# Kernel optimization log

Hardware: AMD Instinct MI355X
Metric: run time of the kernel (lower is better)

The kernel has to match this reference:

```python
import jax, jax.numpy as jnp
import numpy as np

B, L = 1, 384
D_EDGE, D_BIAS, N_HEAD, D_HEAD = 128, 64, 4, 48
INF = 1000000.0
SCALE = 1.0 / np.sqrt(D_HEAD)
EPS = 1e-5


def _layernorm(x, g, b):
    mu = jnp.mean(x, axis=-1, keepdims=True)
    var = jnp.mean(jnp.square(x - mu), axis=-1, keepdims=True)
    return (x - mu) * jax.lax.rsqrt(var + EPS) * g + b


def _rope(x, pos):
    # x: [B, n, L, h, d], pos: [B, L] integer positions along the attended (i/j) axis
    half = x.shape[-1] // 2
    inv_freq = 1.0 / (10000.0 ** (jnp.arange(half, dtype=jnp.float32) / half))
    ang = pos.astype(jnp.float32)[..., None] * inv_freq          # [B, L, half]
    cos = jnp.cos(ang)[:, None, :, None, :]                       # [B,1,L,1,half]
    sin = jnp.sin(ang)[:, None, :, None, :]
    x1, x2 = jnp.split(x, 2, axis=-1)
    return jnp.concatenate([x1 * cos - x2 * sin, x1 * sin + x2 * cos], axis=-1)


def setup_inputs() -> dict:
    key = jax.random.key(0)
    ks = jax.random.split(key, 10)
    s = 0.02
    return {
        "edge": jax.random.normal(ks[0], (B, L, L, D_EDGE), jnp.float32),
        "bias": jax.random.normal(ks[1], (B, L, L, D_BIAS), jnp.float32),
        "edge_pos": jnp.arange(B * L, dtype=jnp.int32).reshape(B, L),
        "edge_mask": jnp.ones((B, L, L), jnp.float32),
        "ln_e_g": jnp.ones((D_EDGE,), jnp.float32),
        "ln_e_b": jnp.zeros((D_EDGE,), jnp.float32),
        "ln_b_g": jnp.ones((D_BIAS,), jnp.float32),
        "ln_b_b": jnp.zeros((D_BIAS,), jnp.float32),
        "Wq": jax.random.normal(ks[2], (D_EDGE, N_HEAD * D_HEAD), jnp.float32) * s,
        "Wk": jax.random.normal(ks[3], (D_EDGE, N_HEAD * D_HEAD), jnp.float32) * s,
        "Wv": jax.random.normal(ks[4], (D_EDGE, N_HEAD * D_HEAD), jnp.float32) * s,
        "Wb": jax.random.normal(ks[5], (D_BIAS, N_HEAD), jnp.float32) * s,
        "Wg": jax.random.normal(ks[6], (D_EDGE, N_HEAD * D_HEAD), jnp.float32) * s,
        "bg": jnp.zeros((N_HEAD * D_HEAD,), jnp.float32),
        "Wo": jax.random.normal(ks[7], (N_HEAD * D_HEAD, D_EDGE), jnp.float32) * s,
    }


def reference(edge, bias, edge_pos, edge_mask, ln_e_g, ln_e_b, ln_b_g, ln_b_b,
              Wq, Wk, Wv, Wb, Wg, bg, Wo):
    # is_row=True: swap the two residue axes of the pair representation
    e = jnp.transpose(edge, (0, 2, 1, 3))
    bi = jnp.transpose(bias, (0, 2, 1, 3))
    e = _layernorm(e, ln_e_g, ln_e_b)
    bi = _layernorm(bi, ln_b_g, ln_b_b)

    def proj(x, W):
        return (x @ W).reshape(B, L, L, N_HEAD, D_HEAD)

    q = proj(e, Wq)                      # [B, n, i, h, d]
    k = proj(e, Wk)
    v = proj(e, Wv)
    q = _rope(q, edge_pos)
    k = _rope(k, edge_pos)
    b_h = bi @ Wb                        # [B, i, j, h]
    gate = jax.nn.sigmoid(proj(e, Wg) + bg.reshape(1, 1, 1, N_HEAD, D_HEAD))

    q = q * SCALE
    k = k / L
    attn = jnp.einsum('bnihk,bnjhk->bijh', q, k) + b_h
    attn = jax.nn.softmax(attn, axis=-2)                 # softmax over j (dim -2)
    attn = attn + (INF * (edge_mask - 1.0))[..., None]    # post-softmax additive mask

    out = jnp.einsum('bijh,bnjhd->bnihd', attn, v)        # [B, n, i, h, d]
    out = gate * out
    out = out.reshape(B, L, L, N_HEAD * D_HEAD) @ Wo      # [B, n, i, d_edge]
    return jnp.transpose(out, (0, 2, 1, 3))               # undo row permute
```

## Files before the change

kernel.cpp:

```cpp
#include <hip/hip_runtime.h>
#include <hip/hip_bf16.h>


#define LQ 384
#define DE 128
#define DBI 64
#define NH 4
#define DH 48
#define NPOS (LQ*LQ)
#define KQK (LQ*DH)

typedef __attribute__((ext_vector_type(8))) short short8;
typedef __attribute__((ext_vector_type(4))) float f32x4;
typedef unsigned short u16;
typedef unsigned int u32;

__device__ __forceinline__ float b2f(u16 u) {
  union { u32 i; float f; } v; v.i = ((u32)u) << 16; return v.f;
}
__device__ __forceinline__ u16 f2b(float f) {
  __hip_bfloat16 h = __float2bfloat16(f);
  return __builtin_bit_cast(unsigned short, h);
}
__device__ __forceinline__ float wred_sum(float v) {
  #pragma unroll
  for (int o = 32; o; o >>= 1) v += __shfl_down(v, o);
  return __shfl(v, 0);
}

__device__ __forceinline__ void gemm_128x192(
    const u16* __restrict__ A, long lda, const u16* __restrict__ B, long ldb,
    int kTiles, u16* sA, u16* sB, f32x4 (&acc)[4][6])
{
  const int t = threadIdx.x;
  const int w = t >> 6, lane = t & 63, quad = lane >> 4, l16 = lane & 15;
  const int wr = w >> 1, wc = w & 1;
  for (int kt = 0; kt < kTiles; ++kt) {
    #pragma unroll
    for (int r = 0; r < 4; ++r) {
      int id = t + r * 256, row = id >> 3, c8 = (id & 7) * 8;
      *(uint4*)(sA + row * 72 + c8) = *(const uint4*)(A + (long)row * lda + kt * 64 + c8);
    }
    #pragma unroll
    for (int r = 0; r < 6; ++r) {
      int id = t + r * 256, row = id >> 3, c8 = (id & 7) * 8;
      *(uint4*)(sB + row * 72 + c8) = *(const uint4*)(B + (long)row * ldb + kt * 64 + c8);
    }
    __syncthreads();
    #pragma unroll
    for (int kk = 0; kk < 64; kk += 32) {
      short8 a[4], bf[6];
      #pragma unroll
      for (int rr = 0; rr < 4; ++rr)
        a[rr] = *(const short8*)(sA + (wr * 64 + rr * 16 + l16) * 72 + kk + quad * 8);
      #pragma unroll
      for (int f = 0; f < 6; ++f)
        bf[f] = *(const short8*)(sB + (wc * 96 + f * 16 + l16) * 72 + kk + quad * 8);
      #pragma unroll
      for (int rr = 0; rr < 4; ++rr)
        #pragma unroll
        for (int f = 0; f < 6; ++f)
          acc[rr][f] = __builtin_amdgcn_mfma_f32_16x16x32_bf16(a[rr], bf[f], acc[rr][f], 0, 0, 0);
    }
    __syncthreads();
  }
}

__global__ __launch_bounds__(256) void k_prep_w(
    const float* __restrict__ Wq, const float* __restrict__ Wk,
    const float* __restrict__ Wv, const float* __restrict__ Wg,
    const float* __restrict__ Wo, const int* __restrict__ epos,
    u16* __restrict__ WT, u16* __restrict__ WoT,
    float* __restrict__ cosT, float* __restrict__ sinT)
{
  int idx = blockIdx.x * 256 + threadIdx.x;
  if (idx < 768 * 128) {
    int col = idx >> 7, c = idx & 127;
    int which = col / 192, wi = col % 192;
    const float* W = (which == 0) ? Wq : (which == 1) ? Wk : (which == 2) ? Wv : Wg;
    WT[(long)col * 128 + c] = f2b(W[(long)c * 192 + wi]);
  }
  if (idx < 128 * 192) {
    int c = idx / 192, col = idx % 192;
    WoT[(long)c * 192 + col] = f2b(Wo[(long)col * 128 + c]);
  }
  if (idx < 384 * 24) {
    int i2 = idx / 24, dd = idx % 24;
    float ang = (float)epos[i2] * exp2f((float)dd * (-13.287712379549449f / 24.f));
    cosT[idx] = cosf(ang);
    sinT[idx] = sinf(ang);
  }
}

__global__ __launch_bounds__(256) void k_ln_e(
    const float* __restrict__ edge, const float* __restrict__ g,
    const float* __restrict__ b, u16* __restrict__ e_ln)
{
  int w = threadIdx.x >> 6, lane = threadIdx.x & 63;
  long p = (long)blockIdx.x * 4 + w;
  int n = (int)(p / LQ), i2 = (int)(p % LQ);
  const float* src = edge + ((long)i2 * LQ + n) * DE;
  float2 x = *(const float2*)(src + lane * 2);
  float mu = wred_sum(x.x + x.y) * (1.f / 128.f);
  float ms = wred_sum(x.x * x.x + x.y * x.y) * (1.f / 128.f);
  float r = rsqrtf(ms - mu * mu + 1e-5f);
  int c = lane * 2;
  u16 y0 = f2b((x.x - mu) * r * g[c] + b[c]);
  u16 y1 = f2b((x.y - mu) * r * g[c + 1] + b[c + 1]);
  *(u32*)(e_ln + p * DE + c) = (u32)y0 | ((u32)y1 << 16);
}

__global__ __launch_bounds__(256) void k_bias(
    const float* __restrict__ bias, const float* __restrict__ g,
    const float* __restrict__ b, const float* __restrict__ Wb,
    float* __restrict__ bh)
{
  int w = threadIdx.x >> 6, lane = threadIdx.x & 63;
  long q = (long)blockIdx.x * 4 + w;
  int i = (int)(q / LQ), j = (int)(q % LQ);
  float x = bias[((long)j * LQ + i) * DBI + lane];
  float mu = wred_sum(x) * (1.f / 64.f);
  float ms = wred_sum(x * x) * (1.f / 64.f);
  float r = rsqrtf(ms - mu * mu + 1e-5f);
  float y = (x - mu) * r * g[lane] + b[lane];
  #pragma unroll
  for (int h = 0; h < 4; ++h) {
    float v = y * Wb[lane * 4 + h];
    #pragma unroll
    for (int o = 32; o; o >>= 1) v += __shfl_down(v, o);
    if (lane == 0) bh[((long)h * LQ + i) * LQ + j] = v;
  }
}

__global__ __launch_bounds__(256) void k_proj(
    const u16* __restrict__ e_ln, const u16* __restrict__ WT,
    const float* __restrict__ cosT, const float* __restrict__ sinT,
    const float* __restrict__ bg,
    u16* __restrict__ q48, u16* __restrict__ k48,
    u16* __restrict__ vT, u16* __restrict__ gate3)
{
  __shared__ __align__(16) u16 sA[128 * 136];
  __shared__ __align__(16) u16 sB[48 * 136];
  __shared__ __align__(16) float sC[128 * 49];
  const int t = threadIdx.x;
  const int w = t >> 6, lane = t & 63, quad = lane >> 4, l16 = lane & 15;
  long mt = blockIdx.x;
  long pbase = mt * 128;
  int n = (int)(pbase / LQ), i2base = (int)(pbase % LQ);

  #pragma unroll
  for (int r = 0; r < 8; ++r) {
    int id = t + r * 256, row = id >> 4, c8 = (id & 15) * 8;
    *(uint4*)(sA + row * 136 + c8) = *(const uint4*)(e_ln + (pbase + row) * DE + c8);
  }
  __syncthreads();
  short8 a[2][4];
  #pragma unroll
  for (int rr = 0; rr < 2; ++rr)
    #pragma unroll
    for (int kki = 0; kki < 4; ++kki)
      a[rr][kki] = *(const short8*)(sA + (w * 32 + rr * 16 + l16) * 136 + kki * 32 + quad * 8);

  for (int cc = 0; cc < 16; ++cc) {
    int which = cc >> 2, h = cc & 3;
    #pragma unroll
    for (int r = 0; r < 3; ++r) {
      int id = t + r * 256, row = id >> 4, c8 = (id & 15) * 8;
      *(uint4*)(sB + row * 136 + c8) = *(const uint4*)(WT + ((long)cc * 48 + row) * DE + c8);
    }
    __syncthreads();
    f32x4 acc[2][3] = {};
    #pragma unroll
    for (int kki = 0; kki < 4; ++kki)
      #pragma unroll
      for (int f = 0; f < 3; ++f) {
        short8 bf = *(const short8*)(sB + (f * 16 + l16) * 136 + kki * 32 + quad * 8);
        acc[0][f] = __builtin_amdgcn_mfma_f32_16x16x32_bf16(a[0][kki], bf, acc[0][f], 0, 0, 0);
        acc[1][f] = __builtin_amdgcn_mfma_f32_16x16x32_bf16(a[1][kki], bf, acc[1][f], 0, 0, 0);
      }
    #pragma unroll
    for (int rr = 0; rr < 2; ++rr)
      #pragma unroll
      for (int f = 0; f < 3; ++f)
        #pragma unroll
        for (int r = 0; r < 4; ++r)
          sC[(w * 32 + rr * 16 + quad * 4 + r) * 49 + f * 16 + l16] = acc[rr][f][r];
    __syncthreads();

    if (which < 2) {
      float scl = (which == 0) ? 0.14433756729740643f : (1.0f / 384.0f);
      u16* base = ((which == 0) ? q48 : k48) + ((long)(h * LQ + n) * LQ + i2base) * DH;
      #pragma unroll
      for (int it = 0; it < 3; ++it) {
        int id = t + it * 256;
        int row = id / 6, c8 = (id % 6) * 8;
        int i2 = i2base + row;
        const float* ct = cosT + i2 * 24;
        const float* st = sinT + i2 * 24;
        union { u16 s[8]; uint4 v; } o;
        #pragma unroll
        for (int u = 0; u < 8; ++u) {
          int d = c8 + u;
          int dd = (d < 24) ? d : d - 24;
          float x1 = sC[row * 49 + dd], x2 = sC[row * 49 + dd + 24];
          float y = (d < 24) ? (x1 * ct[dd] - x2 * st[dd]) : (x1 * st[dd] + x2 * ct[dd]);
          o.s[u] = f2b(y * scl);
        }
        *(uint4*)(base + (long)row * DH + c8) = o.v;
      }
    } else if (which == 2) {
      #pragma unroll
      for (int it = 0; it < 3; ++it) {
        int id = t + it * 256;
        int d = id >> 4, j8 = (id & 15) * 8;
        union { u16 s[8]; uint4 v; } o;
        #pragma unroll
        for (int u = 0; u < 8; ++u) o.s[u] = f2b(sC[(j8 + u) * 49 + d]);
        *(uint4*)(vT + ((long)h * KQK + n * DH + d) * LQ + i2base + j8) = o.v;
      }
    } else {
      #pragma unroll
      for (int it = 0; it < 3; ++it) {
        int id = t + it * 256;
        int row = id / 6, c8 = (id % 6) * 8;
        union { u16 s[8]; uint4 v; } o;
        #pragma unroll
        for (int u = 0; u < 8; ++u) {
          int d = c8 + u;
          float xx = sC[row * 49 + d] + bg[h * DH + d];
          o.s[u] = f2b(1.f / (1.f + __expf(-xx)));
        }
        *(uint4*)(gate3 + ((long)h * NPOS + pbase + row) * DH + c8) = o.v;
      }
    }
  }
}

__global__ __launch_bounds__(256) void k_qk(
    const u16* __restrict__ q48, const u16* __restrict__ k48,
    float* __restrict__ partial)
{
  __shared__ __align__(16) u16 sA[128 * 104];
  __shared__ __align__(16) u16 sB[192 * 104];
  int nt = blockIdx.x & 1, s = blockIdx.x >> 1;
  int mt = blockIdx.y, h = blockIdx.z;
  const int t = threadIdx.x;
  const int w = t >> 6, lane = t & 63, quad = lane >> 4, l16 = lane & 15;
  const int wr = w >> 1, wc = w & 1;
  f32x4 acc[4][6] = {};
  for (int kt = 0; kt < 12; ++kt) {
    int n0 = s * 24 + kt * 2;
    #pragma unroll
    for (int r = 0; r < 6; ++r) {
      int p = r / 3;
      int rem = t + (r - p * 3) * 256;
      int row = rem / 6, c8 = (rem % 6) * 8;
      *(uint4*)(sA + row * 104 + p * 48 + c8) =
        *(const uint4*)(q48 + (((long)h * LQ + n0 + p) * LQ + mt * 128 + row) * DH + c8);
    }
    #pragma unroll
    for (int r = 0; r < 9; ++r) {
      int id = t + r * 256;
      int p = (id >= 1152) ? 1 : 0;
      int rem = id - p * 1152;
      int row = rem / 6, c8 = (rem % 6) * 8;
      *(uint4*)(sB + row * 104 + p * 48 + c8) =
        *(const uint4*)(k48 + (((long)h * LQ + n0 + p) * LQ + nt * 192 + row) * DH + c8);
    }
    __syncthreads();
    #pragma unroll
    for (int kk = 0; kk < 96; kk += 32) {
      short8 a[4], bf[6];
      #pragma unroll
      for (int rr = 0; rr < 4; ++rr)
        a[rr] = *(const short8*)(sA + (wr * 64 + rr * 16 + l16) * 104 + kk + quad * 8);
      #pragma unroll
      for (int f = 0; f < 6; ++f)
        bf[f] = *(const short8*)(sB + (wc * 96 + f * 16 + l16) * 104 + kk + quad * 8);
      #pragma unroll
      for (int rr = 0; rr < 4; ++rr)
        #pragma unroll
        for (int f = 0; f < 6; ++f)
          acc[rr][f] = __builtin_amdgcn_mfma_f32_16x16x32_bf16(a[rr], bf[f], acc[rr][f], 0, 0, 0);
    }
    __syncthreads();
  }
  float* dst = partial + ((long)s * NH + h) * NPOS;
  #pragma unroll
  for (int rr = 0; rr < 4; ++rr)
    #pragma unroll
    for (int f = 0; f < 6; ++f)
      #pragma unroll
      for (int r = 0; r < 4; ++r) {
        int row = mt * 128 + wr * 64 + rr * 16 + quad * 4 + r;
        int col = nt * 192 + wc * 96 + f * 16 + l16;
        dst[(long)row * LQ + col] = acc[rr][f][r];
      }
}

__global__ __launch_bounds__(256) void k_softmax(
    const float* __restrict__ partial, const float* __restrict__ bh,
    const float* __restrict__ mask, u16* __restrict__ attn)
{
  int w = threadIdx.x >> 6, lane = threadIdx.x & 63;
  long row = (long)blockIdx.x * 4 + w;
  int i = (int)(row % LQ);
  float v[6];
  #pragma unroll
  for (int j0 = 0; j0 < 6; ++j0) v[j0] = bh[row * LQ + lane + j0 * 64];
  for (int s = 0; s < 16; ++s) {
    const float* p = partial + (long)s * NH * NPOS + row * LQ;
    #pragma unroll
    for (int j0 = 0; j0 < 6; ++j0) v[j0] += p[lane + j0 * 64];
  }
  float mx = -1e30f;
  #pragma unroll
  for (int j0 = 0; j0 < 6; ++j0) mx = fmaxf(mx, v[j0]);
  #pragma unroll
  for (int o = 32; o; o >>= 1) mx = fmaxf(mx, __shfl_down(mx, o));
  mx = __shfl(mx, 0);
  float sum = 0.f;
  #pragma unroll
  for (int j0 = 0; j0 < 6; ++j0) { v[j0] = __expf(v[j0] - mx); sum += v[j0]; }
  sum = wred_sum(sum);
  float inv = 1.f / sum;
  #pragma unroll
  for (int j0 = 0; j0 < 6; ++j0) {
    int j = lane + j0 * 64;
    float p = v[j0] * inv + 1.0e6f * (mask[(long)i * LQ + j] - 1.f);
    attn[row * LQ + j] = f2b(p);
  }
}

__global__ __launch_bounds__(256) void k_av(
    const u16* __restrict__ attn, const u16* __restrict__ vT,
    u16* __restrict__ out3)
{
  __shared__ __align__(16) u16 sA[128 * 72];
  __shared__ __align__(16) u16 sB[192 * 72];
  int nt = blockIdx.x, h = blockIdx.y;
  const int t = threadIdx.x;
  const int w = t >> 6, lane = t & 63, quad = lane >> 4, l16 = lane & 15;
  const int wr = w >> 1, wc = w & 1;
  for (int mt = 0; mt < 3; ++mt) {
    f32x4 acc[4][6] = {};
    gemm_128x192(attn + ((long)h * LQ + mt * 128) * LQ, LQ,
                 vT + ((long)h * KQK + nt * 192) * LQ, LQ,
                 6, sA, sB, acc);
    u16* sCb = sB;
    #pragma unroll
    for (int ch = 0; ch < 2; ++ch) {
      if (wc == ch) {
        #pragma unroll
        for (int rr = 0; rr < 4; ++rr)
          #pragma unroll
          for (int f = 0; f < 6; ++f)
            #pragma unroll
            for (int r = 0; r < 4; ++r)
              sCb[(wr * 64 + rr * 16 + quad * 4 + r) * 104 + f * 16 + l16] = f2b(acc[rr][f][r]);
      }
      __syncthreads();
      #pragma unroll
      for (int r2 = 0; r2 < 6; ++r2) {
        int id = t + r2 * 256;
        int row = id / 12, u = id % 12;
        int nnl = u / 6, c8 = (u % 6) * 8;
        int nval = nt * 4 + ch * 2 + nnl;
        *(uint4*)(out3 + ((long)h * NPOS + (long)nval * LQ + mt * 128 + row) * DH + c8) =
          *(const uint4*)(sCb + row * 104 + nnl * 48 + c8);
      }
      __syncthreads();
    }
  }
}

__global__ __launch_bounds__(256) void k_out(
    const u16* __restrict__ out3, const u16* __restrict__ gate3,
    const u16* __restrict__ WoT, float* __restrict__ outp)
{
  __shared__ __align__(16) u16 sA[128 * 104];
  __shared__ __align__(16) u16 sB[128 * 104];
  long mt = blockIdx.x;
  long pbase = mt * 128;
  const int t = threadIdx.x;
  const int w = t >> 6, lane = t & 63, quad = lane >> 4, l16 = lane & 15;
  const int wr = w >> 1, wc = w & 1;
  f32x4 acc[4][4] = {};
  for (int kt = 0; kt < 2; ++kt) {
    #pragma unroll
    for (int r = 0; r < 6; ++r) {
      int p = r / 3;
      int rem = t + (r - p * 3) * 256;
      int row = rem / 6, c8 = (rem % 6) * 8;
      long off = ((long)(kt * 2 + p) * NPOS + pbase + row) * DH + c8;
      union { u16 s[8]; uint4 v; } ua, ub, ur;
      ua.v = *(const uint4*)(out3 + off);
      ub.v = *(const uint4*)(gate3 + off);
      #pragma unroll
      for (int q2 = 0; q2 < 8; ++q2) ur.s[q2] = f2b(b2f(ua.s[q2]) * b2f(ub.s[q2]));
      *(uint4*)(sA + row * 104 + p * 48 + c8) = ur.v;
    }
    #pragma unroll
    for (int r = 0; r < 6; ++r) {
      int p = r / 3;
      int rem = t + (r - p * 3) * 256;
      int row = rem / 6, c8 = (rem % 6) * 8;
      *(uint4*)(sB + row * 104 + p * 48 + c8) =
        *(const uint4*)(WoT + (long)row * 192 + kt * 96 + p * 48 + c8);
    }
    __syncthreads();
    #pragma unroll
    for (int kk = 0; kk < 96; kk += 32) {
      short8 a[4], bf[4];
      #pragma unroll
      for (int rr = 0; rr < 4; ++rr)
        a[rr] = *(const short8*)(sA + (wr * 64 + rr * 16 + l16) * 104 + kk + quad * 8);
      #pragma unroll
      for (int f = 0; f < 4; ++f)
        bf[f] = *(const short8*)(sB + (wc * 64 + f * 16 + l16) * 104 + kk + quad * 8);
      #pragma unroll
      for (int rr = 0; rr < 4; ++rr)
        #pragma unroll
        for (int f = 0; f < 4; ++f)
          acc[rr][f] = __builtin_amdgcn_mfma_f32_16x16x32_bf16(a[rr], bf[f], acc[rr][f], 0, 0, 0);
    }
    __syncthreads();
  }
  int n = (int)(pbase / LQ), ibase = (int)(pbase % LQ);
  float* sAf = (float*)sA;
  #pragma unroll
  for (int pass = 0; pass < 4; ++pass) {
    if (wr == (pass >> 1)) {
      #pragma unroll
      for (int rr2 = 0; rr2 < 2; ++rr2) {
        int rr = (pass & 1) * 2 + rr2;
        #pragma unroll
        for (int f = 0; f < 4; ++f)
          #pragma unroll
          for (int r = 0; r < 4; ++r)
            sAf[(rr2 * 16 + quad * 4 + r) * 132 + wc * 64 + f * 16 + l16] = acc[rr][f][r];
      }
    }
    __syncthreads();
    #pragma unroll
    for (int r2 = 0; r2 < 4; ++r2) {
      int id = t + r2 * 256;
      int row32 = id >> 5, c4 = id & 31;
      float4 v = *(const float4*)(sAf + row32 * 132 + c4 * 4);
      *(float4*)(outp + ((long)(ibase + pass * 32 + row32) * LQ + n) * DE + c4 * 4) = v;
    }
    __syncthreads();
  }
}

extern "C" void kernel_launch(void* const* d_in, const int* in_sizes, int n_in,
                              void* d_out, int out_size, void* d_ws, size_t ws_size,
                              hipStream_t stream)
{
  const float* edge   = (const float*)d_in[0];
  const float* bias   = (const float*)d_in[1];
  const int*   epos   = (const int*)d_in[2];
  const float* mask   = (const float*)d_in[3];
  const float* ln_e_g = (const float*)d_in[4];
  const float* ln_e_b = (const float*)d_in[5];
  const float* ln_b_g = (const float*)d_in[6];
  const float* ln_b_b = (const float*)d_in[7];
  const float* Wq = (const float*)d_in[8];
  const float* Wk = (const float*)d_in[9];
  const float* Wv = (const float*)d_in[10];
  const float* Wb = (const float*)d_in[11];
  const float* Wg = (const float*)d_in[12];
  const float* bg = (const float*)d_in[13];
  const float* Wo = (const float*)d_in[14];
  float* outp = (float*)d_out;

  char* ws = (char*)d_ws;
  const size_t SZ = (size_t)NPOS * 192 * 2;
  u16* e_ln      = (u16*)ws;
  float* partial = (float*)ws;
  u16* out3      = (u16*)ws;
  u16* q48   = (u16*)(ws + SZ);
  u16* k48   = (u16*)(ws + 2 * SZ);
  u16* vTb   = (u16*)(ws + 3 * SZ);
  u16* gate3 = (u16*)(ws + 4 * SZ);
  float* bh  = (float*)(ws + 5 * SZ);
  u16* attn  = (u16*)(ws + 5 * SZ + 2359296);
  u16* WT    = (u16*)(ws + 5 * SZ + 2359296 + 1179648);
  u16* WoT   = (u16*)(ws + 5 * SZ + 2359296 + 1179648 + 196608);
  float* cosT = (float*)(ws + 5 * SZ + 2359296 + 1179648 + 196608 + 49152);
  float* sinT = cosT + 384 * 24;

  k_prep_w<<<dim3(384), dim3(256), 0, stream>>>(Wq, Wk, Wv, Wg, Wo, epos, WT, WoT, cosT, sinT);
  k_bias<<<dim3(36864), dim3(256), 0, stream>>>(bias, ln_b_g, ln_b_b, Wb, bh);
  k_ln_e<<<dim3(36864), dim3(256), 0, stream>>>(edge, ln_e_g, ln_e_b, e_ln);
  k_proj<<<dim3(1152), dim3(256), 0, stream>>>(e_ln, WT, cosT, sinT, bg,
                                               q48, k48, vTb, gate3);
  k_qk<<<dim3(32, 3, 4), dim3(256), 0, stream>>>(q48, k48, partial);
  k_softmax<<<dim3(384), dim3(256), 0, stream>>>(partial, bh, mask, attn);
  k_av<<<dim3(96, 4), dim3(256), 0, stream>>>(attn, vTb, out3);
  k_out<<<dim3(1152), dim3(256), 0, stream>>>(out3, gate3, WoT, outp);
}
```

Measured before the change: 642.6 us.

## Replace block-wide barriers with per-wave LDS staging in proj, av, out epilogues

```diff
diff --git a/kernel.cpp b/kernel.cpp
--- a/kernel.cpp
+++ b/kernel.cpp
@@ -14,6 +14,8 @@
 typedef __attribute__((ext_vector_type(4))) float f32x4;
 typedef unsigned short u16;
 typedef unsigned int u32;
+
+#define LFENCE() asm volatile("s_waitcnt lgkmcnt(0)" ::: "memory")
 
 __device__ __forceinline__ float b2f(u16 u) {
   union { u32 i; float f; } v; v.i = ((u32)u) << 16; return v.f;
@@ -139,98 +141,115 @@
     u16* __restrict__ q48, u16* __restrict__ k48,
     u16* __restrict__ vT, u16* __restrict__ gate3)
 {
-  __shared__ __align__(16) u16 sA[128 * 136];
-  __shared__ __align__(16) u16 sB[48 * 136];
-  __shared__ __align__(16) float sC[128 * 49];
+  __shared__ __align__(16) char sR[4][7936];
   const int t = threadIdx.x;
   const int w = t >> 6, lane = t & 63, quad = lane >> 4, l16 = lane & 15;
   long mt = blockIdx.x;
   long pbase = mt * 128;
   int n = (int)(pbase / LQ), i2base = (int)(pbase % LQ);
 
-  #pragma unroll
-  for (int r = 0; r < 8; ++r) {
-    int id = t + r * 256, row = id >> 4, c8 = (id & 15) * 8;
-    *(uint4*)(sA + row * 136 + c8) = *(const uint4*)(e_ln + (pbase + row) * DE + c8);
-  }
-  __syncthreads();
   short8 a[2][4];
   #pragma unroll
   for (int rr = 0; rr < 2; ++rr)
     #pragma unroll
     for (int kki = 0; kki < 4; ++kki)
-      a[rr][kki] = *(const short8*)(sA + (w * 32 + rr * 16 + l16) * 136 + kki * 32 + quad * 8);
+      a[rr][kki] = *(const short8*)(e_ln + (pbase + w * 32 + rr * 16 + l16) * DE + kki * 32 + quad * 8);
+
+  const int row = lane >> 1, half = lane & 1;
+  const int i2 = i2base + w * 32 + row;
+  char* R = sR[w];
 
   for (int cc = 0; cc < 16; ++cc) {
     int which = cc >> 2, h = cc & 3;
-    #pragma unroll
-    for (int r = 0; r < 3; ++r) {
-      int id = t + r * 256, row = id >> 4, c8 = (id & 15) * 8;
-      *(uint4*)(sB + row * 136 + c8) = *(const uint4*)(WT + ((long)cc * 48 + row) * DE + c8);
-    }
-    __syncthreads();
+    short8 b[3][4];
+    #pragma unroll
+    for (int f = 0; f < 3; ++f)
+      #pragma unroll
+      for (int kki = 0; kki < 4; ++kki)
+        b[f][kki] = *(const short8*)(WT + ((long)cc * 48 + f * 16 + l16) * DE + kki * 32 + quad * 8);
     f32x4 acc[2][3] = {};
     #pragma unroll
     for (int kki = 0; kki < 4; ++kki)
       #pragma unroll
       for (int f = 0; f < 3; ++f) {
-        short8 bf = *(const short8*)(sB + (f * 16 + l16) * 136 + kki * 32 + quad * 8);
-        acc[0][f] = __builtin_amdgcn_mfma_f32_16x16x32_bf16(a[0][kki], bf, acc[0][f], 0, 0, 0);
-        acc[1][f] = __builtin_amdgcn_mfma_f32_16x16x32_bf16(a[1][kki], bf, acc[1][f], 0, 0, 0);
+        acc[0][f] = __builtin_amdgcn_mfma_f32_16x16x32_bf16(a[0][kki], b[f][kki], acc[0][f], 0, 0, 0);
+        acc[1][f] = __builtin_amdgcn_mfma_f32_16x16x32_bf16(a[1][kki], b[f][kki], acc[1][f], 0, 0, 0);
       }
-    #pragma unroll
-    for (int rr = 0; rr < 2; ++rr)
-      #pragma unroll
-      for (int f = 0; f < 3; ++f)
-        #pragma unroll
-        for (int r = 0; r < 4; ++r)
-          sC[(w * 32 + rr * 16 + quad * 4 + r) * 49 + f * 16 + l16] = acc[rr][f][r];
-    __syncthreads();
+    LFENCE();
 
     if (which < 2) {
+      float* Rf = (float*)R;
+      #pragma unroll
+      for (int rr = 0; rr < 2; ++rr)
+        #pragma unroll
+        for (int f = 0; f < 3; ++f)
+          #pragma unroll
+          for (int r = 0; r < 4; ++r)
+            Rf[(rr * 16 + quad * 4 + r) * 60 + f * 16 + l16] = acc[rr][f][r];
+      LFENCE();
+      float own[24], oth[24], cs[24], sn[24];
+      #pragma unroll
+      for (int e4 = 0; e4 < 6; ++e4) {
+        float4 v1 = *(const float4*)(Rf + row * 60 + half * 24 + e4 * 4);
+        float4 v2 = *(const float4*)(Rf + row * 60 + (1 - half) * 24 + e4 * 4);
+        float4 c1 = *(const float4*)(cosT + i2 * 24 + e4 * 4);
+        float4 s1 = *(const float4*)(sinT + i2 * 24 + e4 * 4);
+        own[e4*4+0]=v1.x; own[e4*4+1]=v1.y; own[e4*4+2]=v1.z; own[e4*4+3]=v1.w;
+        oth[e4*4+0]=v2.x; oth[e4*4+1]=v2.y; oth[e4*4+2]=v2.z; oth[e4*4+3]=v2.w;
+        cs[e4*4+0]=c1.x; cs[e4*4+1]=c1.y; cs[e4*4+2]=c1.z; cs[e4*4+3]=c1.w;
+        sn[e4*4+0]=s1.x; sn[e4*4+1]=s1.y; sn[e4*4+2]=s1.z; sn[e4*4+3]=s1.w;
+      }
       float scl = (which == 0) ? 0.14433756729740643f : (1.0f / 384.0f);
-      u16* base = ((which == 0) ? q48 : k48) + ((long)(h * LQ + n) * LQ + i2base) * DH;
-      #pragma unroll
-      for (int it = 0; it < 3; ++it) {
-        int id = t + it * 256;
-        int row = id / 6, c8 = (id % 6) * 8;
-        int i2 = i2base + row;
-        const float* ct = cosT + i2 * 24;
-        const float* st = sinT + i2 * 24;
-        union { u16 s[8]; uint4 v; } o;
-        #pragma unroll
-        for (int u = 0; u < 8; ++u) {
-          int d = c8 + u;
-          int dd = (d < 24) ? d : d - 24;
-          float x1 = sC[row * 49 + dd], x2 = sC[row * 49 + dd + 24];
-          float y = (d < 24) ? (x1 * ct[dd] - x2 * st[dd]) : (x1 * st[dd] + x2 * ct[dd]);
-          o.s[u] = f2b(y * scl);
+      float sgn = half ? 1.f : -1.f;
+      u16* dst = ((which == 0) ? q48 : k48) + ((long)(h * LQ + n) * LQ + i2) * 48 + half * 24;
+      #pragma unroll
+      for (int v3 = 0; v3 < 3; ++v3) {
+        union { u16 s[8]; uint4 q; } o;
+        #pragma unroll
+        for (int j = 0; j < 8; ++j) {
+          int e = v3 * 8 + j;
+          o.s[j] = f2b((own[e] * cs[e] + sgn * oth[e] * sn[e]) * scl);
         }
-        *(uint4*)(base + (long)row * DH + c8) = o.v;
+        *(uint4*)(dst + v3 * 8) = o.q;
       }
     } else if (which == 2) {
+      u16* Ru = (u16*)R;
+      #pragma unroll
+      for (int rr = 0; rr < 2; ++rr)
+        #pragma unroll
+        for (int f = 0; f < 3; ++f)
+          #pragma unroll
+          for (int r = 0; r < 4; ++r)
+            Ru[(f * 16 + l16) * 40 + rr * 16 + quad * 4 + r] = f2b(acc[rr][f][r]);
+      LFENCE();
       #pragma unroll
       for (int it = 0; it < 3; ++it) {
-        int id = t + it * 256;
-        int d = id >> 4, j8 = (id & 15) * 8;
-        union { u16 s[8]; uint4 v; } o;
-        #pragma unroll
-        for (int u = 0; u < 8; ++u) o.s[u] = f2b(sC[(j8 + u) * 49 + d]);
-        *(uint4*)(vT + ((long)h * KQK + n * DH + d) * LQ + i2base + j8) = o.v;
+        int id = it * 64 + lane;
+        int d = id >> 2, seg = id & 3;
+        uint4 v = *(const uint4*)(Ru + d * 40 + seg * 8);
+        *(uint4*)(vT + ((long)(h * KQK + n * 48 + d)) * LQ + i2base + w * 32 + seg * 8) = v;
       }
     } else {
-      #pragma unroll
-      for (int it = 0; it < 3; ++it) {
-        int id = t + it * 256;
-        int row = id / 6, c8 = (id % 6) * 8;
-        union { u16 s[8]; uint4 v; } o;
-        #pragma unroll
-        for (int u = 0; u < 8; ++u) {
-          int d = c8 + u;
-          float xx = sC[row * 49 + d] + bg[h * DH + d];
-          o.s[u] = f2b(1.f / (1.f + __expf(-xx)));
+      u16* Ru = (u16*)R;
+      #pragma unroll
+      for (int rr = 0; rr < 2; ++rr)
+        #pragma unroll
+        for (int f = 0; f < 3; ++f)
+          #pragma unroll
+          for (int r = 0; r < 4; ++r)
+            Ru[(rr * 16 + quad * 4 + r) * 56 + f * 16 + l16] = f2b(acc[rr][f][r]);
+      LFENCE();
+      u16* dst = gate3 + ((long)h * NPOS + pbase + w * 32 + row) * 48 + half * 24;
+      #pragma unroll
+      for (int v3 = 0; v3 < 3; ++v3) {
+        union { u16 s[8]; uint4 q; } iv, o;
+        iv.q = *(const uint4*)(Ru + row * 56 + half * 24 + v3 * 8);
+        #pragma unroll
+        for (int j = 0; j < 8; ++j) {
+          float x = b2f(iv.s[j]) + bg[h * 48 + half * 24 + v3 * 8 + j];
+          o.s[j] = f2b(1.f / (1.f + __expf(-x)));
         }
-        *(uint4*)(gate3 + ((long)h * NPOS + pbase + row) * DH + c8) = o.v;
+        *(uint4*)(dst + v3 * 8) = o.q;
       }
     }
   }
@@ -292,9 +311,9 @@
     for (int f = 0; f < 6; ++f)
       #pragma unroll
       for (int r = 0; r < 4; ++r) {
-        int row = mt * 128 + wr * 64 + rr * 16 + quad * 4 + r;
+        int rowc = mt * 128 + wr * 64 + rr * 16 + quad * 4 + r;
         int col = nt * 192 + wc * 96 + f * 16 + l16;
-        dst[(long)row * LQ + col] = acc[rr][f][r];
+        dst[(long)rowc * LQ + col] = acc[rr][f][r];
       }
 }
 
@@ -342,35 +361,31 @@
   const int t = threadIdx.x;
   const int w = t >> 6, lane = t & 63, quad = lane >> 4, l16 = lane & 15;
   const int wr = w >> 1, wc = w & 1;
+  const int plane = lane >> 5, row16 = (lane >> 1) & 15, half = lane & 1;
   for (int mt = 0; mt < 3; ++mt) {
     f32x4 acc[4][6] = {};
     gemm_128x192(attn + ((long)h * LQ + mt * 128) * LQ, LQ,
                  vT + ((long)h * KQK + nt * 192) * LQ, LQ,
                  6, sA, sB, acc);
-    u16* sCb = sB;
-    #pragma unroll
-    for (int ch = 0; ch < 2; ++ch) {
-      if (wc == ch) {
-        #pragma unroll
-        for (int rr = 0; rr < 4; ++rr)
-          #pragma unroll
-          for (int f = 0; f < 6; ++f)
-            #pragma unroll
-            for (int r = 0; r < 4; ++r)
-              sCb[(wr * 64 + rr * 16 + quad * 4 + r) * 104 + f * 16 + l16] = f2b(acc[rr][f][r]);
-      }
-      __syncthreads();
-      #pragma unroll
-      for (int r2 = 0; r2 < 6; ++r2) {
-        int id = t + r2 * 256;
-        int row = id / 12, u = id % 12;
-        int nnl = u / 6, c8 = (u % 6) * 8;
-        int nval = nt * 4 + ch * 2 + nnl;
-        *(uint4*)(out3 + ((long)h * NPOS + (long)nval * LQ + mt * 128 + row) * DH + c8) =
-          *(const uint4*)(sCb + row * 104 + nnl * 48 + c8);
-      }
-      __syncthreads();
-    }
+    u16* R = (u16*)((char*)sA + w * 4608);
+    #pragma unroll
+    for (int rr = 0; rr < 4; ++rr) {
+      LFENCE();
+      #pragma unroll
+      for (int f = 0; f < 6; ++f)
+        #pragma unroll
+        for (int r = 0; r < 4; ++r)
+          R[(quad * 4 + r) * 104 + f * 16 + l16] = f2b(acc[rr][f][r]);
+      LFENCE();
+      int nn = nt * 4 + wc * 2 + plane;
+      int i = mt * 128 + wr * 64 + rr * 16 + row16;
+      const u16* src = R + row16 * 104 + plane * 48 + half * 24;
+      u16* dst = out3 + ((long)h * NPOS + (long)nn * LQ + i) * 48 + half * 24;
+      *(uint4*)(dst)      = *(const uint4*)(src);
+      *(uint4*)(dst + 8)  = *(const uint4*)(src + 8);
+      *(uint4*)(dst + 16) = *(const uint4*)(src + 16);
+    }
+    if (mt != 2) __syncthreads();
   }
 }
 
@@ -427,29 +442,23 @@
     __syncthreads();
   }
   int n = (int)(pbase / LQ), ibase = (int)(pbase % LQ);
-  float* sAf = (float*)sA;
-  #pragma unroll
-  for (int pass = 0; pass < 4; ++pass) {
-    if (wr == (pass >> 1)) {
-      #pragma unroll
-      for (int rr2 = 0; rr2 < 2; ++rr2) {
-        int rr = (pass & 1) * 2 + rr2;
-        #pragma unroll
-        for (int f = 0; f < 4; ++f)
-          #pragma unroll
-          for (int r = 0; r < 4; ++r)
-            sAf[(rr2 * 16 + quad * 4 + r) * 132 + wc * 64 + f * 16 + l16] = acc[rr][f][r];
-      }
-    }
-    __syncthreads();
-    #pragma unroll
-    for (int r2 = 0; r2 < 4; ++r2) {
-      int id = t + r2 * 256;
-      int row32 = id >> 5, c4 = id & 31;
-      float4 v = *(const float4*)(sAf + row32 * 132 + c4 * 4);
-      *(float4*)(outp + ((long)(ibase + pass * 32 + row32) * LQ + n) * DE + c4 * 4) = v;
-    }
-    __syncthreads();
+  float* R = (float*)((char*)sB + w * 6656);
+  const int row16 = lane >> 2, q4 = lane & 3;
+  #pragma unroll
+  for (int rr = 0; rr < 4; ++rr) {
+    LFENCE();
+    #pragma unroll
+    for (int f = 0; f < 4; ++f)
+      #pragma unroll
+      for (int r = 0; r < 4; ++r)
+        R[(quad * 4 + r) * 68 + f * 16 + l16] = acc[rr][f][r];
+    LFENCE();
+    int i = ibase + wr * 64 + rr * 16 + row16;
+    float* dst = outp + ((long)i * LQ + n) * DE + wc * 64 + q4 * 16;
+    const float* src = R + row16 * 68 + q4 * 16;
+    #pragma unroll
+    for (int v = 0; v < 4; ++v)
+      *(float4*)(dst + v * 4) = *(const float4*)(src + v * 4);
   }
 }
 
```

Measured after the change: 579.0 us. -9.9%, faster.
